# Performance work log

Hardware: AMD Instinct MI355X
Metric: run time of the kernel (lower is better)

## Reference

```python
import jax, jax.numpy as jnp
import numpy as np

B, C, H, W = 4, 64, 256, 256
HEADS, DHEAD = 4, 64
INNER = HEADS * DHEAD


def setup_inputs() -> dict:
    key = jax.random.key(0)
    ks = jax.random.split(key, 8)
    s = 1.0 / np.sqrt(C)
    return {
        "x_in": jax.random.normal(ks[0], (B, C, H, W), jnp.float32),
        "illu_fea_trans": jax.random.normal(ks[1], (B, C, H, W), jnp.float32),
        "Wq": jax.random.normal(ks[2], (C, INNER), jnp.float32) * s,
        "Wk": jax.random.normal(ks[3], (C, INNER), jnp.float32) * s,
        "Wv": jax.random.normal(ks[4], (C, INNER), jnp.float32) * s,
        "WL": jax.random.normal(ks[5], (C, INNER), jnp.float32) * s,
        "rescale": jnp.ones((HEADS, 1, 1), jnp.float32),
        "Wp": jax.random.normal(ks[6], (INNER, C), jnp.float32) / np.sqrt(INNER),
        "bp": jnp.zeros((C,), jnp.float32),
    }


def _l2norm(t, axis=-1, eps=1e-12):
    # matches torch F.normalize(p=2): x / max(||x||, eps)
    n = jnp.sqrt(jnp.sum(t * t, axis=axis, keepdims=True))
    return t / jnp.maximum(n, eps)


def reference(x_in, illu_fea_trans, Wq, Wk, Wv, WL, rescale, Wp, bp):
    b, c, h, w = x_in.shape
    n = h * w
    # NCHW -> [b, n, c]
    x = jnp.transpose(x_in, (0, 2, 3, 1)).reshape(b, n, c)
    illu = jnp.transpose(illu_fea_trans, (0, 2, 3, 1)).reshape(b, n, c)

    def split_heads(t):  # [b,n,inner] -> [b,heads,d,n] (transposed attention)
        return jnp.transpose(t.reshape(b, n, HEADS, DHEAD), (0, 2, 3, 1))

    q = split_heads(x @ Wq)           # [b,h,d,n]
    k = split_heads(x @ Wk)
    v = split_heads(x @ Wv) * split_heads(illu @ WL)  # illumination-gated v

    q = _l2norm(q, axis=-1)
    k = _l2norm(k, axis=-1)
    attn = jnp.einsum('bhdn,bhen->bhde', k, q)  # [b,h,d,d]
    attn = jax.nn.softmax(attn * rescale[None], axis=-1)
    out = jnp.einsum('bhde,bhen->bhdn', attn, v)  # [b,h,d,n]

    # [b,h,d,n] -> [b,n,inner]
    out = jnp.transpose(out, (0, 3, 1, 2)).reshape(b, n, INNER)
    out = out @ Wp + bp  # [b,n,c]
    return jnp.transpose(out.reshape(b, h, w, c), (0, 3, 1, 2))  # [b,c,h,w]
```

## Files before the change

### kernel.cpp

```cpp
#include <hip/hip_runtime.h>
#include <hip/hip_bf16.h>


#define NPOS 65536
#define CH 64
#define INNER 256

typedef __attribute__((ext_vector_type(8))) __bf16 bfrag;
typedef __attribute__((ext_vector_type(4))) float facc;
typedef __attribute__((ext_vector_type(4))) float fvec4;

__device__ __forceinline__ unsigned short f2bu(float f) {
  return __builtin_bit_cast(unsigned short, (__bf16)f);
}

#define SWA(row, colbyte) ((row) * 128 + ((colbyte) ^ (((row) & 7) << 4)))

__global__ __launch_bounds__(256) void k0_wt(const float* __restrict__ Wv,
                                             const float* __restrict__ WL,
                                             unsigned short* __restrict__ WvT,
                                             unsigned short* __restrict__ WLT) {
  int t = blockIdx.x * 256 + threadIdx.x;
  int c = t >> 8, i = t & 255;
  WvT[i * CH + c] = f2bu(Wv[c * INNER + i]);
  WLT[i * CH + c] = f2bu(WL[c * INNER + i]);
}

__global__ __launch_bounds__(256) void k1_xx(const float* __restrict__ x,
                                             float* __restrict__ xx) {
  const int b = blockIdx.y;
  const int wave = threadIdx.x >> 6, lane = threadIdx.x & 63;
  const int r = lane & 15, g = lane >> 4;
  const int gw = blockIdx.x * 4 + wave;
  const int per = NPOS / 128;
  const size_t n0 = (size_t)gw * per;
  const float* xb = x + (size_t)b * CH * NPOS;

  facc acc[4][4] = {};

  for (int n = 0; n < per; n += 32) {
    bfrag fr[4];
#pragma unroll
    for (int t = 0; t < 4; ++t) {
      const float* p = xb + (size_t)(16 * t + r) * NPOS + n0 + n + g * 8;
      fvec4 lo = *(const fvec4*)p;
      fvec4 hi = *(const fvec4*)(p + 4);
      bfrag f;
#pragma unroll
      for (int e = 0; e < 4; ++e) { f[e] = (__bf16)lo[e]; f[e + 4] = (__bf16)hi[e]; }
      fr[t] = f;
    }
#pragma unroll
    for (int ti = 0; ti < 4; ++ti)
#pragma unroll
      for (int tj = 0; tj < 4; ++tj)
        acc[ti][tj] = __builtin_amdgcn_mfma_f32_16x16x32_bf16(fr[ti], fr[tj],
                                                              acc[ti][tj], 0, 0, 0);
  }

  __shared__ float red[4][4096];
  float* my = red[wave];
#pragma unroll
  for (int ti = 0; ti < 4; ++ti)
#pragma unroll
    for (int tj = 0; tj < 4; ++tj)
#pragma unroll
      for (int q = 0; q < 4; ++q)
        my[(16 * ti + g * 4 + q) * 64 + 16 * tj + r] = acc[ti][tj][q];
  __syncthreads();
  float* xxb = xx + (size_t)b * 4096;
  for (int i = threadIdx.x; i < 4096; i += 256)
    atomicAdd(xxb + i, red[0][i] + red[1][i] + red[2][i] + red[3][i]);
}

__global__ __launch_bounds__(256) void k2_attn(
    const float* __restrict__ xx, const float* __restrict__ Wq,
    const float* __restrict__ Wk, const float* __restrict__ rescale,
    const float* __restrict__ Wp, unsigned short* __restrict__ Mt) {
  const int b = blockIdx.x >> 2, h = blockIdx.x & 3;
  const int t = threadIdx.x;
  const int wave = t >> 6, lane = t & 63;
  const int r = lane & 15, g = lane >> 4;

  __shared__ __align__(16) char tXX[8192];
  __shared__ __align__(16) char tWq[8192];
  __shared__ __align__(16) char tWk[8192];
  __shared__ __align__(16) char tWp[8192];
  __shared__ __align__(16) char tZq[8192];
  __shared__ __align__(16) char tZk[8192];
  __shared__ __align__(16) char tAt[8192];
  __shared__ float gG[64][68];
  __shared__ float sMx[64][4], sSm[64][4];
  __shared__ float sNq[64], sNk[64];

  const float* xxb = xx + (size_t)b * 4096;
#pragma unroll
  for (int rep = 0; rep < 16; ++rep) {
    int idx = rep * 256 + t;
    int row = idx >> 6, col = idx & 63;
    *(unsigned short*)(tXX + SWA(row, col * 2)) = f2bu(xxb[idx]);
    float vq = Wq[row * INNER + h * 64 + col];
    float vk = Wk[row * INNER + h * 64 + col];
    *(unsigned short*)(tWq + SWA(col, row * 2)) = f2bu(vq);
    *(unsigned short*)(tWk + SWA(col, row * 2)) = f2bu(vk);
    *(unsigned short*)(tWp + SWA(col, row * 2)) = f2bu(Wp[(h * 64 + row) * CH + col]);
  }
  __syncthreads();

  facc zq[4] = {}, zk[4] = {};
#pragma unroll
  for (int s = 0; s < 2; ++s) {
    bfrag aq = *(const bfrag*)(tWq + SWA(16 * wave + r, s * 64 + g * 16));
    bfrag ak = *(const bfrag*)(tWk + SWA(16 * wave + r, s * 64 + g * 16));
#pragma unroll
    for (int tj = 0; tj < 4; ++tj) {
      bfrag bx = *(const bfrag*)(tXX + SWA(16 * tj + r, s * 64 + g * 16));
      zq[tj] = __builtin_amdgcn_mfma_f32_16x16x32_bf16(aq, bx, zq[tj], 0, 0, 0);
      zk[tj] = __builtin_amdgcn_mfma_f32_16x16x32_bf16(ak, bx, zk[tj], 0, 0, 0);
    }
  }
#pragma unroll
  for (int tj = 0; tj < 4; ++tj)
#pragma unroll
    for (int q = 0; q < 4; ++q) {
      int row = 16 * wave + g * 4 + q, colb = (16 * tj + r) * 2;
      *(unsigned short*)(tZq + SWA(row, colb)) = f2bu(zq[tj][q]);
      *(unsigned short*)(tZk + SWA(row, colb)) = f2bu(zk[tj][q]);
    }
  __syncthreads();

  facc ga[4] = {}, q2[4] = {}, k2[4] = {};
#pragma unroll
  for (int s = 0; s < 2; ++s) {
    bfrag azk = *(const bfrag*)(tZk + SWA(16 * wave + r, s * 64 + g * 16));
    bfrag azq = *(const bfrag*)(tZq + SWA(16 * wave + r, s * 64 + g * 16));
#pragma unroll
    for (int tj = 0; tj < 4; ++tj) {
      bfrag bq = *(const bfrag*)(tWq + SWA(16 * tj + r, s * 64 + g * 16));
      bfrag bk = *(const bfrag*)(tWk + SWA(16 * tj + r, s * 64 + g * 16));
      ga[tj] = __builtin_amdgcn_mfma_f32_16x16x32_bf16(azk, bq, ga[tj], 0, 0, 0);
      q2[tj] = __builtin_amdgcn_mfma_f32_16x16x32_bf16(azq, bq, q2[tj], 0, 0, 0);
      k2[tj] = __builtin_amdgcn_mfma_f32_16x16x32_bf16(azk, bk, k2[tj], 0, 0, 0);
    }
  }
#pragma unroll
  for (int tj = 0; tj < 4; ++tj)
#pragma unroll
    for (int q = 0; q < 4; ++q) {
      int row = 16 * wave + g * 4 + q, col = 16 * tj + r;
      gG[row][col] = ga[tj][q];
      if (row == col) { sNq[row] = q2[tj][q]; sNk[row] = k2[tj][q]; }
    }
  __syncthreads();

  if (t < 64) {
    sNq[t] = 1.f / fmaxf(sqrtf(sNq[t]), 1e-12f);
    sNk[t] = rescale[h] / fmaxf(sqrtf(sNk[t]), 1e-12f);
  }
  __syncthreads();

  {
    const int d = t >> 2, p = t & 3;
    const float ik = sNk[d];
    float le[16];
    float mx = -1e30f;
#pragma unroll
    for (int j = 0; j < 16; ++j) {
      float v = gG[d][16 * p + j] * ik * sNq[16 * p + j];
      le[j] = v; mx = fmaxf(mx, v);
    }
    sMx[d][p] = mx;
    __syncthreads();
    mx = fmaxf(fmaxf(sMx[d][0], sMx[d][1]), fmaxf(sMx[d][2], sMx[d][3]));
    float sm = 0.f;
#pragma unroll
    for (int j = 0; j < 16; ++j) { le[j] = __expf(le[j] - mx); sm += le[j]; }
    sSm[d][p] = sm;
    __syncthreads();
    sm = sSm[d][0] + sSm[d][1] + sSm[d][2] + sSm[d][3];
    const float inv = 1.f / sm;
#pragma unroll
    for (int j = 0; j < 16; ++j) {
      int e = 16 * p + j;
      *(unsigned short*)(tAt + SWA(e, d * 2)) = f2bu(le[j] * inv);
    }
  }
  __syncthreads();

  facc m[4] = {};
#pragma unroll
  for (int s = 0; s < 2; ++s) {
    bfrag aa = *(const bfrag*)(tAt + SWA(16 * wave + r, s * 64 + g * 16));
#pragma unroll
    for (int tj = 0; tj < 4; ++tj) {
      bfrag bw = *(const bfrag*)(tWp + SWA(16 * tj + r, s * 64 + g * 16));
      m[tj] = __builtin_amdgcn_mfma_f32_16x16x32_bf16(aa, bw, m[tj], 0, 0, 0);
    }
  }
#pragma unroll
  for (int tj = 0; tj < 4; ++tj)
#pragma unroll
    for (int q = 0; q < 4; ++q) {
      int e = 16 * wave + g * 4 + q, c2 = 16 * tj + r;
      Mt[((size_t)(b * CH + c2)) * INNER + h * 64 + e] = f2bu(m[tj][q]);
    }
}

__global__ __launch_bounds__(256) void k3_out(
    const float* __restrict__ x, const float* __restrict__ illu,
    const unsigned short* __restrict__ WvT, const unsigned short* __restrict__ WLT,
    const unsigned short* __restrict__ Mt, const float* __restrict__ bp,
    float* __restrict__ out) {
  const int b = blockIdx.y;
  const int wave = threadIdx.x >> 6, lane = threadIdx.x & 63;
  const int r = lane & 15, g = lane >> 4;
  const int n0 = blockIdx.x * 256;

  __shared__ __align__(16) char lxs[8192];
  __shared__ __align__(16) char lis[8192];
  __shared__ __align__(16) char lvs[2][8192];

  bfrag wvA[4][2], wlA[4][2], mtA[8];
#pragma unroll
  for (int ti = 0; ti < 4; ++ti) {
    const int i = wave * 64 + ti * 16 + r;
#pragma unroll
    for (int s = 0; s < 2; ++s) {
      wvA[ti][s] = *(const bfrag*)(WvT + i * CH + s * 32 + g * 8);
      wlA[ti][s] = *(const bfrag*)(WLT + i * CH + s * 32 + g * 8);
    }
  }
#pragma unroll
  for (int s8 = 0; s8 < 8; ++s8)
    mtA[s8] = *(const bfrag*)(Mt + ((size_t)(b * CH + wave * 16 + r)) * INNER + s8 * 32 + g * 8);
  float bcol[4];
#pragma unroll
  for (int q = 0; q < 4; ++q) bcol[q] = bp[wave * 16 + g * 4 + q];

  const float* xb = x + (size_t)b * CH * NPOS;
  const float* ib = illu + (size_t)b * CH * NPOS;
  float* ob = out + (size_t)b * CH * NPOS;

  const int sc2 = threadIdx.x >> 3;
  const int sjo = (threadIdx.x & 7) * 8;

  for (int chunk = 0; chunk < 4; ++chunk) {
    const int nbase = n0 + chunk * 64;
    {
      const float* px0 = xb + (size_t)(2 * sc2) * NPOS + nbase + sjo;
      const float* pi0 = ib + (size_t)(2 * sc2) * NPOS + nbase + sjo;
      fvec4 xa0 = *(const fvec4*)px0,          xa1 = *(const fvec4*)(px0 + 4);
      fvec4 xb0 = *(const fvec4*)(px0 + NPOS), xb1 = *(const fvec4*)(px0 + NPOS + 4);
      fvec4 ia0 = *(const fvec4*)pi0,          ia1 = *(const fvec4*)(pi0 + 4);
      fvec4 ib0 = *(const fvec4*)(pi0 + NPOS), ib1 = *(const fvec4*)(pi0 + NPOS + 4);
#pragma unroll
      for (int jj = 0; jj < 8; ++jj) {
        const int j = sjo + jj;
        const int byte = (sc2 * 4) ^ (((j ^ (j >> 3)) & 7) << 4);
        float x0 = jj < 4 ? xa0[jj & 3] : xa1[jj & 3];
        float x1 = jj < 4 ? xb0[jj & 3] : xb1[jj & 3];
        float i0 = jj < 4 ? ia0[jj & 3] : ia1[jj & 3];
        float i1 = jj < 4 ? ib0[jj & 3] : ib1[jj & 3];
        *(unsigned int*)(lxs + j * 128 + byte) =
            (unsigned int)f2bu(x0) | ((unsigned int)f2bu(x1) << 16);
        *(unsigned int*)(lis + j * 128 + byte) =
            (unsigned int)f2bu(i0) | ((unsigned int)f2bu(i1) << 16);
      }
    }
    __syncthreads();

#pragma unroll
    for (int sub = 0; sub < 4; ++sub) {
      const int vb = sub & 1;
      const int j0 = sub * 16;
      const int j = j0 + r;
      const int swv = ((j ^ (j >> 3)) & 7) << 4;
      bfrag xB[2], iB[2];
#pragma unroll
      for (int s = 0; s < 2; ++s) {
        const int byte = (s * 64 + g * 16) ^ swv;
        xB[s] = *(const bfrag*)(lxs + j * 128 + byte);
        iB[s] = *(const bfrag*)(lis + j * 128 + byte);
      }
      facc av[4] = {}, gv[4] = {};
#pragma unroll
      for (int ti = 0; ti < 4; ++ti) {
#pragma unroll
        for (int s = 0; s < 2; ++s) {
          av[ti] = __builtin_amdgcn_mfma_f32_16x16x32_bf16(wvA[ti][s], xB[s], av[ti], 0, 0, 0);
          gv[ti] = __builtin_amdgcn_mfma_f32_16x16x32_bf16(wlA[ti][s], iB[s], gv[ti], 0, 0, 0);
        }
      }
#pragma unroll
      for (int ti = 0; ti < 4; ++ti) {
        const float v0 = av[ti][0] * gv[ti][0], v1 = av[ti][1] * gv[ti][1];
        const float v2 = av[ti][2] * gv[ti][2], v3 = av[ti][3] * gv[ti][3];
        const int i = wave * 64 + ti * 16 + g * 4;
        const int sw = (r & 7) << 4;
        *(unsigned int*)(lvs[vb] + r * 512 + ((i * 2) ^ sw)) =
            (unsigned int)f2bu(v0) | ((unsigned int)f2bu(v1) << 16);
        *(unsigned int*)(lvs[vb] + r * 512 + (((i + 2) * 2) ^ sw)) =
            (unsigned int)f2bu(v2) | ((unsigned int)f2bu(v3) << 16);
      }
      __syncthreads();
      facc ov = {0.f, 0.f, 0.f, 0.f};
#pragma unroll
      for (int s8 = 0; s8 < 8; ++s8) {
        const int byte = (s8 * 64 + g * 16) ^ ((r & 7) << 4);
        bfrag vB = *(const bfrag*)(lvs[vb] + r * 512 + byte);
        ov = __builtin_amdgcn_mfma_f32_16x16x32_bf16(mtA[s8], vB, ov, 0, 0, 0);
      }
#pragma unroll
      for (int q = 0; q < 4; ++q)
        ob[(size_t)(wave * 16 + g * 4 + q) * NPOS + nbase + j0 + r] = ov[q] + bcol[q];
    }
  }
}

extern "C" void kernel_launch(void* const* d_in, const int* in_sizes, int n_in,
                              void* d_out, int out_size, void* d_ws, size_t ws_size,
                              hipStream_t stream) {
  (void)in_sizes; (void)n_in; (void)out_size; (void)ws_size;
  const float* x    = (const float*)d_in[0];
  const float* illu = (const float*)d_in[1];
  const float* Wq   = (const float*)d_in[2];
  const float* Wk   = (const float*)d_in[3];
  const float* Wv   = (const float*)d_in[4];
  const float* WL   = (const float*)d_in[5];
  const float* rsc  = (const float*)d_in[6];
  const float* Wp   = (const float*)d_in[7];
  const float* bp   = (const float*)d_in[8];
  float* out = (float*)d_out;

  float* xxws = (float*)d_ws;
  unsigned short* Mt  = (unsigned short*)((char*)d_ws + 65536);
  unsigned short* WvT = (unsigned short*)((char*)d_ws + 65536 + 131072);
  unsigned short* WLT = WvT + INNER * CH;

  hipMemsetAsync(d_ws, 0, (size_t)4 * 4096 * sizeof(float), stream);
  hipLaunchKernelGGL(k0_wt, dim3(64), dim3(256), 0, stream, Wv, WL, WvT, WLT);
  hipLaunchKernelGGL(k1_xx, dim3(32, 4), dim3(256), 0, stream, x, xxws);
  hipLaunchKernelGGL(k2_attn, dim3(16), dim3(256), 0, stream, xxws, Wq, Wk, rsc, Wp, Mt);
  hipLaunchKernelGGL(k3_out, dim3(256, 4), dim3(256), 0, stream, x, illu, WvT, WLT, Mt, bp, out);
}
```

Measured before the change: 83.96 us.

## Double-buffer x/illu staging in k3_out with register prefetch and MFMA priority

```diff
diff --git a/kernel.cpp b/kernel.cpp
--- a/kernel.cpp
+++ b/kernel.cpp
@@ -206,7 +206,7 @@
     }
 }
 
-__global__ __launch_bounds__(256) void k3_out(
+__global__ __launch_bounds__(256, 3) void k3_out(
     const float* __restrict__ x, const float* __restrict__ illu,
     const unsigned short* __restrict__ WvT, const unsigned short* __restrict__ WLT,
     const unsigned short* __restrict__ Mt, const float* __restrict__ bp,
@@ -216,8 +216,8 @@
   const int r = lane & 15, g = lane >> 4;
   const int n0 = blockIdx.x * 256;
 
-  __shared__ __align__(16) char lxs[8192];
-  __shared__ __align__(16) char lis[8192];
+  __shared__ __align__(16) char lxs[2][8192];
+  __shared__ __align__(16) char lis[2][8192];
   __shared__ __align__(16) char lvs[2][8192];
 
   bfrag wvA[4][2], wlA[4][2], mtA[8];
@@ -244,30 +244,43 @@
   const int sc2 = threadIdx.x >> 3;
   const int sjo = (threadIdx.x & 7) * 8;
 
+  fvec4 xa0, xa1, xr0, xr1, ia0, ia1, ir0, ir1;
+
+#define LOADC(NB)                                                         \
+  {                                                                       \
+    const float* px0 = xb + (size_t)(2 * sc2) * NPOS + (NB) + sjo;        \
+    const float* pi0 = ib + (size_t)(2 * sc2) * NPOS + (NB) + sjo;        \
+    xa0 = *(const fvec4*)px0;          xa1 = *(const fvec4*)(px0 + 4);    \
+    xr0 = *(const fvec4*)(px0 + NPOS); xr1 = *(const fvec4*)(px0 + NPOS + 4); \
+    ia0 = *(const fvec4*)pi0;          ia1 = *(const fvec4*)(pi0 + 4);    \
+    ir0 = *(const fvec4*)(pi0 + NPOS); ir1 = *(const fvec4*)(pi0 + NPOS + 4); \
+  }
+
+#define WRITEC(BUF)                                                       \
+  {                                                                       \
+    _Pragma("unroll")                                                     \
+    for (int jj = 0; jj < 8; ++jj) {                                      \
+      const int j = sjo + jj;                                             \
+      const int byte = (sc2 * 4) ^ (((j ^ (j >> 3)) & 7) << 4);           \
+      float x0 = jj < 4 ? xa0[jj & 3] : xa1[jj & 3];                      \
+      float x1 = jj < 4 ? xr0[jj & 3] : xr1[jj & 3];                      \
+      float i0 = jj < 4 ? ia0[jj & 3] : ia1[jj & 3];                      \
+      float i1 = jj < 4 ? ir0[jj & 3] : ir1[jj & 3];                      \
+      *(unsigned int*)(lxs[BUF] + j * 128 + byte) =                       \
+          (unsigned int)f2bu(x0) | ((unsigned int)f2bu(x1) << 16);        \
+      *(unsigned int*)(lis[BUF] + j * 128 + byte) =                       \
+          (unsigned int)f2bu(i0) | ((unsigned int)f2bu(i1) << 16);        \
+    }                                                                     \
+  }
+
+  LOADC(n0);
+  WRITEC(0);
+  __syncthreads();
+
   for (int chunk = 0; chunk < 4; ++chunk) {
+    const int cb = chunk & 1;
     const int nbase = n0 + chunk * 64;
-    {
-      const float* px0 = xb + (size_t)(2 * sc2) * NPOS + nbase + sjo;
-      const float* pi0 = ib + (size_t)(2 * sc2) * NPOS + nbase + sjo;
-      fvec4 xa0 = *(const fvec4*)px0,          xa1 = *(const fvec4*)(px0 + 4);
-      fvec4 xb0 = *(const fvec4*)(px0 + NPOS), xb1 = *(const fvec4*)(px0 + NPOS + 4);
-      fvec4 ia0 = *(const fvec4*)pi0,          ia1 = *(const fvec4*)(pi0 + 4);
-      fvec4 ib0 = *(const fvec4*)(pi0 + NPOS), ib1 = *(const fvec4*)(pi0 + NPOS + 4);
-#pragma unroll
-      for (int jj = 0; jj < 8; ++jj) {
-        const int j = sjo + jj;
-        const int byte = (sc2 * 4) ^ (((j ^ (j >> 3)) & 7) << 4);
-        float x0 = jj < 4 ? xa0[jj & 3] : xa1[jj & 3];
-        float x1 = jj < 4 ? xb0[jj & 3] : xb1[jj & 3];
-        float i0 = jj < 4 ? ia0[jj & 3] : ia1[jj & 3];
-        float i1 = jj < 4 ? ib0[jj & 3] : ib1[jj & 3];
-        *(unsigned int*)(lxs + j * 128 + byte) =
-            (unsigned int)f2bu(x0) | ((unsigned int)f2bu(x1) << 16);
-        *(unsigned int*)(lis + j * 128 + byte) =
-            (unsigned int)f2bu(i0) | ((unsigned int)f2bu(i1) << 16);
-      }
-    }
-    __syncthreads();
+    if (chunk < 3) LOADC(nbase + 64);
 
 #pragma unroll
     for (int sub = 0; sub < 4; ++sub) {
@@ -279,10 +292,11 @@
 #pragma unroll
       for (int s = 0; s < 2; ++s) {
         const int byte = (s * 64 + g * 16) ^ swv;
-        xB[s] = *(const bfrag*)(lxs + j * 128 + byte);
-        iB[s] = *(const bfrag*)(lis + j * 128 + byte);
+        xB[s] = *(const bfrag*)(lxs[cb] + j * 128 + byte);
+        iB[s] = *(const bfrag*)(lis[cb] + j * 128 + byte);
       }
       facc av[4] = {}, gv[4] = {};
+      __builtin_amdgcn_s_setprio(1);
 #pragma unroll
       for (int ti = 0; ti < 4; ++ti) {
 #pragma unroll
@@ -291,6 +305,7 @@
           gv[ti] = __builtin_amdgcn_mfma_f32_16x16x32_bf16(wlA[ti][s], iB[s], gv[ti], 0, 0, 0);
         }
       }
+      __builtin_amdgcn_s_setprio(0);
 #pragma unroll
       for (int ti = 0; ti < 4; ++ti) {
         const float v0 = av[ti][0] * gv[ti][0], v1 = av[ti][1] * gv[ti][1];
@@ -304,17 +319,24 @@
       }
       __syncthreads();
       facc ov = {0.f, 0.f, 0.f, 0.f};
+      __builtin_amdgcn_s_setprio(1);
 #pragma unroll
       for (int s8 = 0; s8 < 8; ++s8) {
         const int byte = (s8 * 64 + g * 16) ^ ((r & 7) << 4);
         bfrag vB = *(const bfrag*)(lvs[vb] + r * 512 + byte);
         ov = __builtin_amdgcn_mfma_f32_16x16x32_bf16(mtA[s8], vB, ov, 0, 0, 0);
       }
+      __builtin_amdgcn_s_setprio(0);
 #pragma unroll
       for (int q = 0; q < 4; ++q)
         ob[(size_t)(wave * 16 + g * 4 + q) * NPOS + nbase + j0 + r] = ov[q] + bcol[q];
     }
-  }
+
+    if (chunk < 3) WRITEC(cb ^ 1);
+    __syncthreads();
+  }
+#undef LOADC
+#undef WRITEC
 }
 
 extern "C" void kernel_launch(void* const* d_in, const int* in_sizes, int n_in,
```

Result: slower. 208.6 us (+148.5%).

## Restructure output kernel so each wave owns positions and chains MFMA without LDS round-trip

Applied to the files above, without the earlier changes.

```diff
diff --git a/kernel.cpp b/kernel.cpp
--- a/kernel.cpp
+++ b/kernel.cpp
@@ -9,10 +9,22 @@
 typedef __attribute__((ext_vector_type(8))) __bf16 bfrag;
 typedef __attribute__((ext_vector_type(4))) float facc;
 typedef __attribute__((ext_vector_type(4))) float fvec4;
+typedef __attribute__((ext_vector_type(4))) short sh4;
 
 __device__ __forceinline__ unsigned short f2bu(float f) {
   return __builtin_bit_cast(unsigned short, (__bf16)f);
 }
+
+#if __has_builtin(__builtin_amdgcn_mfma_f32_16x16x16bf16_1k)
+__device__ __forceinline__ facc mfma16(sh4 a, sh4 b, facc c) {
+  return __builtin_amdgcn_mfma_f32_16x16x16bf16_1k(a, b, c, 0, 0, 0);
+}
+#else
+__device__ __forceinline__ facc mfma16(sh4 a, sh4 b, facc c) {
+  asm("v_mfma_f32_16x16x16_bf16 %0, %1, %2, %0" : "+v"(c) : "v"(a), "v"(b));
+  return c;
+}
+#endif
 
 #define SWA(row, colbyte) ((row) * 128 + ((colbyte) ^ (((row) & 7) << 4)))
 
@@ -76,7 +88,7 @@
 __global__ __launch_bounds__(256) void k2_attn(
     const float* __restrict__ xx, const float* __restrict__ Wq,
     const float* __restrict__ Wk, const float* __restrict__ rescale,
-    const float* __restrict__ Wp, unsigned short* __restrict__ Mt) {
+    const float* __restrict__ Wp, unsigned short* __restrict__ Mt3) {
   const int b = blockIdx.x >> 2, h = blockIdx.x & 3;
   const int t = threadIdx.x;
   const int wave = t >> 6, lane = t & 63;
@@ -201,118 +213,90 @@
   for (int tj = 0; tj < 4; ++tj)
 #pragma unroll
     for (int q = 0; q < 4; ++q) {
-      int e = 16 * wave + g * 4 + q, c2 = 16 * tj + r;
-      Mt[((size_t)(b * CH + c2)) * INNER + h * 64 + e] = f2bu(m[tj][q]);
+      int i_glob = h * 64 + 16 * wave + g * 4 + q;
+      int c2 = 16 * tj + r;
+      Mt3[((size_t)b * 16 + (i_glob >> 4)) * 1024 + c2 * 16 + (i_glob & 15)] =
+          f2bu(m[tj][q]);
     }
 }
 
 __global__ __launch_bounds__(256) void k3_out(
     const float* __restrict__ x, const float* __restrict__ illu,
     const unsigned short* __restrict__ WvT, const unsigned short* __restrict__ WLT,
-    const unsigned short* __restrict__ Mt, const float* __restrict__ bp,
+    const unsigned short* __restrict__ Mt3, const float* __restrict__ bp,
     float* __restrict__ out) {
   const int b = blockIdx.y;
   const int wave = threadIdx.x >> 6, lane = threadIdx.x & 63;
   const int r = lane & 15, g = lane >> 4;
-  const int n0 = blockIdx.x * 256;
-
-  __shared__ __align__(16) char lxs[8192];
-  __shared__ __align__(16) char lis[8192];
-  __shared__ __align__(16) char lvs[2][8192];
-
-  bfrag wvA[4][2], wlA[4][2], mtA[8];
-#pragma unroll
-  for (int ti = 0; ti < 4; ++ti) {
-    const int i = wave * 64 + ti * 16 + r;
+  const int n0 = blockIdx.x * 256 + wave * 64;
+
+  __shared__ __align__(16) char sst[4][2][2048];
+  char* myx = sst[wave][0];
+  char* myi = sst[wave][1];
+
+  const float* xb = x + (size_t)b * CH * NPOS + (size_t)lane * NPOS;
+  const float* ib = illu + (size_t)b * CH * NPOS + (size_t)lane * NPOS;
+  float* ob = out + (size_t)b * CH * NPOS;
+  const unsigned short* mt = Mt3 + (size_t)b * 16384;
+
+  float bias[4];
+#pragma unroll
+  for (int ct = 0; ct < 4; ++ct) bias[ct] = bp[ct * 16 + r];
+
+  for (int t = 0; t < 4; ++t) {
+    const int nb = n0 + t * 16;
+    {
+      fvec4 xv[4], iv[4];
+#pragma unroll
+      for (int p = 0; p < 4; ++p) {
+        xv[p] = *(const fvec4*)(xb + nb + p * 4);
+        iv[p] = *(const fvec4*)(ib + nb + p * 4);
+      }
+#pragma unroll
+      for (int j = 0; j < 16; ++j) {
+        const int byte = (lane * 2) ^ ((j & 7) << 4);
+        *(unsigned short*)(myx + j * 128 + byte) = f2bu(xv[j >> 2][j & 3]);
+        *(unsigned short*)(myi + j * 128 + byte) = f2bu(iv[j >> 2][j & 3]);
+      }
+    }
+    bfrag xB[2], iB[2];
 #pragma unroll
     for (int s = 0; s < 2; ++s) {
-      wvA[ti][s] = *(const bfrag*)(WvT + i * CH + s * 32 + g * 8);
-      wlA[ti][s] = *(const bfrag*)(WLT + i * CH + s * 32 + g * 8);
-    }
-  }
-#pragma unroll
-  for (int s8 = 0; s8 < 8; ++s8)
-    mtA[s8] = *(const bfrag*)(Mt + ((size_t)(b * CH + wave * 16 + r)) * INNER + s8 * 32 + g * 8);
-  float bcol[4];
-#pragma unroll
-  for (int q = 0; q < 4; ++q) bcol[q] = bp[wave * 16 + g * 4 + q];
-
-  const float* xb = x + (size_t)b * CH * NPOS;
-  const float* ib = illu + (size_t)b * CH * NPOS;
-  float* ob = out + (size_t)b * CH * NPOS;
-
-  const int sc2 = threadIdx.x >> 3;
-  const int sjo = (threadIdx.x & 7) * 8;
-
-  for (int chunk = 0; chunk < 4; ++chunk) {
-    const int nbase = n0 + chunk * 64;
-    {
-      const float* px0 = xb + (size_t)(2 * sc2) * NPOS + nbase + sjo;
-      const float* pi0 = ib + (size_t)(2 * sc2) * NPOS + nbase + sjo;
-      fvec4 xa0 = *(const fvec4*)px0,          xa1 = *(const fvec4*)(px0 + 4);
-      fvec4 xb0 = *(const fvec4*)(px0 + NPOS), xb1 = *(const fvec4*)(px0 + NPOS + 4);
-      fvec4 ia0 = *(const fvec4*)pi0,          ia1 = *(const fvec4*)(pi0 + 4);
-      fvec4 ib0 = *(const fvec4*)(pi0 + NPOS), ib1 = *(const fvec4*)(pi0 + NPOS + 4);
-#pragma unroll
-      for (int jj = 0; jj < 8; ++jj) {
-        const int j = sjo + jj;
-        const int byte = (sc2 * 4) ^ (((j ^ (j >> 3)) & 7) << 4);
-        float x0 = jj < 4 ? xa0[jj & 3] : xa1[jj & 3];
-        float x1 = jj < 4 ? xb0[jj & 3] : xb1[jj & 3];
-        float i0 = jj < 4 ? ia0[jj & 3] : ia1[jj & 3];
-        float i1 = jj < 4 ? ib0[jj & 3] : ib1[jj & 3];
-        *(unsigned int*)(lxs + j * 128 + byte) =
-            (unsigned int)f2bu(x0) | ((unsigned int)f2bu(x1) << 16);
-        *(unsigned int*)(lis + j * 128 + byte) =
-            (unsigned int)f2bu(i0) | ((unsigned int)f2bu(i1) << 16);
+      const int byte = (s * 64 + g * 16) ^ ((r & 7) << 4);
+      xB[s] = *(const bfrag*)(myx + r * 128 + byte);
+      iB[s] = *(const bfrag*)(myi + r * 128 + byte);
+    }
+
+    facc acc[4] = {};
+#pragma unroll 4
+    for (int ti = 0; ti < 16; ++ti) {
+      const int irow = ti * 16 + r;
+      bfrag wv0 = *(const bfrag*)(WvT + irow * CH + g * 8);
+      bfrag wv1 = *(const bfrag*)(WvT + irow * CH + 32 + g * 8);
+      bfrag wl0 = *(const bfrag*)(WLT + irow * CH + g * 8);
+      bfrag wl1 = *(const bfrag*)(WLT + irow * CH + 32 + g * 8);
+      facc av = {}, gv = {};
+      av = __builtin_amdgcn_mfma_f32_16x16x32_bf16(wv0, xB[0], av, 0, 0, 0);
+      av = __builtin_amdgcn_mfma_f32_16x16x32_bf16(wv1, xB[1], av, 0, 0, 0);
+      gv = __builtin_amdgcn_mfma_f32_16x16x32_bf16(wl0, iB[0], gv, 0, 0, 0);
+      gv = __builtin_amdgcn_mfma_f32_16x16x32_bf16(wl1, iB[1], gv, 0, 0, 0);
+      sh4 a2;
+#pragma unroll
+      for (int e = 0; e < 4; ++e)
+        a2[e] = (short)f2bu(av[e] * gv[e]);
+      const unsigned short* mrow = mt + ti * 1024 + g * 4;
+#pragma unroll
+      for (int ct = 0; ct < 4; ++ct) {
+        sh4 mb = *(const sh4*)(mrow + (ct * 16 + r) * 16);
+        acc[ct] = mfma16(a2, mb, acc[ct]);
       }
     }
-    __syncthreads();
-
-#pragma unroll
-    for (int sub = 0; sub < 4; ++sub) {
-      const int vb = sub & 1;
-      const int j0 = sub * 16;
-      const int j = j0 + r;
-      const int swv = ((j ^ (j >> 3)) & 7) << 4;
-      bfrag xB[2], iB[2];
-#pragma unroll
-      for (int s = 0; s < 2; ++s) {
-        const int byte = (s * 64 + g * 16) ^ swv;
-        xB[s] = *(const bfrag*)(lxs + j * 128 + byte);
-        iB[s] = *(const bfrag*)(lis + j * 128 + byte);
-      }
-      facc av[4] = {}, gv[4] = {};
-#pragma unroll
-      for (int ti = 0; ti < 4; ++ti) {
-#pragma unroll
-        for (int s = 0; s < 2; ++s) {
-          av[ti] = __builtin_amdgcn_mfma_f32_16x16x32_bf16(wvA[ti][s], xB[s], av[ti], 0, 0, 0);
-          gv[ti] = __builtin_amdgcn_mfma_f32_16x16x32_bf16(wlA[ti][s], iB[s], gv[ti], 0, 0, 0);
-        }
-      }
-#pragma unroll
-      for (int ti = 0; ti < 4; ++ti) {
-        const float v0 = av[ti][0] * gv[ti][0], v1 = av[ti][1] * gv[ti][1];
-        const float v2 = av[ti][2] * gv[ti][2], v3 = av[ti][3] * gv[ti][3];
-        const int i = wave * 64 + ti * 16 + g * 4;
-        const int sw = (r & 7) << 4;
-        *(unsigned int*)(lvs[vb] + r * 512 + ((i * 2) ^ sw)) =
-            (unsigned int)f2bu(v0) | ((unsigned int)f2bu(v1) << 16);
-        *(unsigned int*)(lvs[vb] + r * 512 + (((i + 2) * 2) ^ sw)) =
-            (unsigned int)f2bu(v2) | ((unsigned int)f2bu(v3) << 16);
-      }
-      __syncthreads();
-      facc ov = {0.f, 0.f, 0.f, 0.f};
-#pragma unroll
-      for (int s8 = 0; s8 < 8; ++s8) {
-        const int byte = (s8 * 64 + g * 16) ^ ((r & 7) << 4);
-        bfrag vB = *(const bfrag*)(lvs[vb] + r * 512 + byte);
-        ov = __builtin_amdgcn_mfma_f32_16x16x32_bf16(mtA[s8], vB, ov, 0, 0, 0);
-      }
-#pragma unroll
-      for (int q = 0; q < 4; ++q)
-        ob[(size_t)(wave * 16 + g * 4 + q) * NPOS + nbase + j0 + r] = ov[q] + bcol[q];
+#pragma unroll
+    for (int ct = 0; ct < 4; ++ct) {
+      fvec4 o;
+#pragma unroll
+      for (int q = 0; q < 4; ++q) o[q] = acc[ct][q] + bias[ct];
+      *(fvec4*)(ob + (size_t)(ct * 16 + r) * NPOS + nb + g * 4) = o;
     }
   }
 }
@@ -333,13 +317,13 @@
   float* out = (float*)d_out;
 
   float* xxws = (float*)d_ws;
-  unsigned short* Mt  = (unsigned short*)((char*)d_ws + 65536);
+  unsigned short* Mt3 = (unsigned short*)((char*)d_ws + 65536);
   unsigned short* WvT = (unsigned short*)((char*)d_ws + 65536 + 131072);
   unsigned short* WLT = WvT + INNER * CH;
 
   hipMemsetAsync(d_ws, 0, (size_t)4 * 4096 * sizeof(float), stream);
   hipLaunchKernelGGL(k0_wt, dim3(64), dim3(256), 0, stream, Wv, WL, WvT, WLT);
   hipLaunchKernelGGL(k1_xx, dim3(32, 4), dim3(256), 0, stream, x, xxws);
-  hipLaunchKernelGGL(k2_attn, dim3(16), dim3(256), 0, stream, xxws, Wq, Wk, rsc, Wp, Mt);
-  hipLaunchKernelGGL(k3_out, dim3(256, 4), dim3(256), 0, stream, x, illu, WvT, WLT, Mt, bp, out);
-}
+  hipLaunchKernelGGL(k2_attn, dim3(16), dim3(256), 0, stream, xxws, Wq, Wk, rsc, Wp, Mt3);
+  hipLaunchKernelGGL(k3_out, dim3(256, 4), dim3(256), 0, stream, x, illu, WvT, WLT, Mt3, bp, out);
+}
```

Measured after the change: 209.2 us. 149% more time.

## Double-buffer k3 input tiles via async global-to-LDS loads

Applied to the files above, without the earlier changes.

```diff
diff --git a/kernel.cpp b/kernel.cpp
--- a/kernel.cpp
+++ b/kernel.cpp
@@ -10,11 +10,18 @@
 typedef __attribute__((ext_vector_type(4))) float facc;
 typedef __attribute__((ext_vector_type(4))) float fvec4;
 
+typedef const __attribute__((address_space(1))) unsigned int guint;
+typedef __attribute__((address_space(3))) unsigned int luint;
+
 __device__ __forceinline__ unsigned short f2bu(float f) {
   return __builtin_bit_cast(unsigned short, (__bf16)f);
 }
 
 #define SWA(row, colbyte) ((row) * 128 + ((colbyte) ^ (((row) & 7) << 4)))
+
+#define BAR_VM4()  asm volatile("s_waitcnt vmcnt(4)\n\ts_barrier" ::: "memory")
+#define BAR_VM0()  asm volatile("s_waitcnt vmcnt(0)\n\ts_barrier" ::: "memory")
+#define BAR_LGKM() asm volatile("s_waitcnt lgkmcnt(0)\n\ts_barrier" ::: "memory")
 
 __global__ __launch_bounds__(256) void k0_wt(const float* __restrict__ Wv,
                                              const float* __restrict__ WL,
@@ -216,8 +223,8 @@
   const int r = lane & 15, g = lane >> 4;
   const int n0 = blockIdx.x * 256;
 
-  __shared__ __align__(16) char lxs[8192];
-  __shared__ __align__(16) char lis[8192];
+  __shared__ __align__(16) float xf[2][64][32];
+  __shared__ __align__(16) float ifl[2][64][32];
   __shared__ __align__(16) char lvs[2][8192];
 
   bfrag wvA[4][2], wlA[4][2], mtA[8];
@@ -241,48 +248,58 @@
   const float* ib = illu + (size_t)b * CH * NPOS;
   float* ob = out + (size_t)b * CH * NPOS;
 
-  const int sc2 = threadIdx.x >> 3;
-  const int sjo = (threadIdx.x & 7) * 8;
-
-  for (int chunk = 0; chunk < 4; ++chunk) {
-    const int nbase = n0 + chunk * 64;
-    {
-      const float* px0 = xb + (size_t)(2 * sc2) * NPOS + nbase + sjo;
-      const float* pi0 = ib + (size_t)(2 * sc2) * NPOS + nbase + sjo;
-      fvec4 xa0 = *(const fvec4*)px0,          xa1 = *(const fvec4*)(px0 + 4);
-      fvec4 xb0 = *(const fvec4*)(px0 + NPOS), xb1 = *(const fvec4*)(px0 + NPOS + 4);
-      fvec4 ia0 = *(const fvec4*)pi0,          ia1 = *(const fvec4*)(pi0 + 4);
-      fvec4 ib0 = *(const fvec4*)(pi0 + NPOS), ib1 = *(const fvec4*)(pi0 + NPOS + 4);
-#pragma unroll
-      for (int jj = 0; jj < 8; ++jj) {
-        const int j = sjo + jj;
-        const int byte = (sc2 * 4) ^ (((j ^ (j >> 3)) & 7) << 4);
-        float x0 = jj < 4 ? xa0[jj & 3] : xa1[jj & 3];
-        float x1 = jj < 4 ? xb0[jj & 3] : xb1[jj & 3];
-        float i0 = jj < 4 ? ia0[jj & 3] : ia1[jj & 3];
-        float i1 = jj < 4 ? ib0[jj & 3] : ib1[jj & 3];
-        *(unsigned int*)(lxs + j * 128 + byte) =
-            (unsigned int)f2bu(x0) | ((unsigned int)f2bu(x1) << 16);
-        *(unsigned int*)(lis + j * 128 + byte) =
-            (unsigned int)f2bu(i0) | ((unsigned int)f2bu(i1) << 16);
-      }
-    }
-    __syncthreads();
-
-#pragma unroll
-    for (int sub = 0; sub < 4; ++sub) {
-      const int vb = sub & 1;
+  const int c0 = wave * 16 + (lane >> 3);
+  const int c1 = c0 + 8;
+  const int k0_ = (c0 >> 3) & 3, k1_ = (c1 >> 3) & 3;
+  const int fk0 = k0_ ^ ((k0_ & 1) << 2), fk1 = k1_ ^ ((k1_ & 1) << 2);
+  const size_t off0 = (size_t)c0 * NPOS + (((lane & 7) ^ fk0) << 2);
+  const size_t off1 = (size_t)c1 * NPOS + (((lane & 7) ^ fk1) << 2);
+
+#define ISSUE(BUF, NC)                                                        \
+  {                                                                           \
+    __builtin_amdgcn_global_load_lds((guint*)(xb + off0 + (NC)),              \
+        (luint*)&xf[BUF][wave * 16][0], 16, 0, 0);                            \
+    __builtin_amdgcn_global_load_lds((guint*)(xb + off1 + (NC)),              \
+        (luint*)&xf[BUF][wave * 16 + 8][0], 16, 0, 0);                        \
+    __builtin_amdgcn_global_load_lds((guint*)(ib + off0 + (NC)),              \
+        (luint*)&ifl[BUF][wave * 16][0], 16, 0, 0);                           \
+    __builtin_amdgcn_global_load_lds((guint*)(ib + off1 + (NC)),              \
+        (luint*)&ifl[BUF][wave * 16 + 8][0], 16, 0, 0);                       \
+  }
+
+  ISSUE(0, n0);
+  BAR_VM0();
+
+  const int fkr = g ^ ((g & 1) << 2);
+
+  for (int cc = 0; cc < 8; ++cc) {
+    const int cb = cc & 1;
+    const int nbase = n0 + cc * 32;
+    if (cc < 7) ISSUE(cb ^ 1, nbase + 32);
+    BAR_VM4();
+
+#pragma unroll 2
+    for (int sub = 0; sub < 2; ++sub) {
       const int j0 = sub * 16;
       const int j = j0 + r;
-      const int swv = ((j ^ (j >> 3)) & 7) << 4;
+      const int qw = ((((j >> 2) ^ fkr) << 2) | (j & 3));
       bfrag xB[2], iB[2];
 #pragma unroll
       for (int s = 0; s < 2; ++s) {
-        const int byte = (s * 64 + g * 16) ^ swv;
-        xB[s] = *(const bfrag*)(lxs + j * 128 + byte);
-        iB[s] = *(const bfrag*)(lis + j * 128 + byte);
+        float xw[8], iw[8];
+#pragma unroll
+        for (int e = 0; e < 8; ++e) {
+          const int c = s * 32 + g * 8 + e;
+          xw[e] = xf[cb][c][qw];
+          iw[e] = ifl[cb][c][qw];
+        }
+        bfrag fx, fi;
+#pragma unroll
+        for (int e = 0; e < 8; ++e) { fx[e] = (__bf16)xw[e]; fi[e] = (__bf16)iw[e]; }
+        xB[s] = fx; iB[s] = fi;
       }
       facc av[4] = {}, gv[4] = {};
+      __builtin_amdgcn_s_setprio(1);
 #pragma unroll
       for (int ti = 0; ti < 4; ++ti) {
 #pragma unroll
@@ -291,30 +308,34 @@
           gv[ti] = __builtin_amdgcn_mfma_f32_16x16x32_bf16(wlA[ti][s], iB[s], gv[ti], 0, 0, 0);
         }
       }
+      __builtin_amdgcn_s_setprio(0);
 #pragma unroll
       for (int ti = 0; ti < 4; ++ti) {
         const float v0 = av[ti][0] * gv[ti][0], v1 = av[ti][1] * gv[ti][1];
         const float v2 = av[ti][2] * gv[ti][2], v3 = av[ti][3] * gv[ti][3];
         const int i = wave * 64 + ti * 16 + g * 4;
         const int sw = (r & 7) << 4;
-        *(unsigned int*)(lvs[vb] + r * 512 + ((i * 2) ^ sw)) =
-            (unsigned int)f2bu(v0) | ((unsigned int)f2bu(v1) << 16);
-        *(unsigned int*)(lvs[vb] + r * 512 + (((i + 2) * 2) ^ sw)) =
-            (unsigned int)f2bu(v2) | ((unsigned int)f2bu(v3) << 16);
+        unsigned long long pk =
+            (unsigned long long)((unsigned int)f2bu(v0) | ((unsigned int)f2bu(v1) << 16)) |
+            ((unsigned long long)((unsigned int)f2bu(v2) | ((unsigned int)f2bu(v3) << 16)) << 32);
+        *(unsigned long long*)(lvs[sub] + r * 512 + ((i * 2) ^ sw)) = pk;
       }
-      __syncthreads();
+      BAR_LGKM();
       facc ov = {0.f, 0.f, 0.f, 0.f};
+      __builtin_amdgcn_s_setprio(1);
 #pragma unroll
       for (int s8 = 0; s8 < 8; ++s8) {
         const int byte = (s8 * 64 + g * 16) ^ ((r & 7) << 4);
-        bfrag vB = *(const bfrag*)(lvs[vb] + r * 512 + byte);
+        bfrag vB = *(const bfrag*)(lvs[sub] + r * 512 + byte);
         ov = __builtin_amdgcn_mfma_f32_16x16x32_bf16(mtA[s8], vB, ov, 0, 0, 0);
       }
+      __builtin_amdgcn_s_setprio(0);
 #pragma unroll
       for (int q = 0; q < 4; ++q)
         ob[(size_t)(wave * 16 + g * 4 + q) * NPOS + nbase + j0 + r] = ov[q] + bcol[q];
     }
   }
+#undef ISSUE
 }
 
 extern "C" void kernel_launch(void* const* d_in, const int* in_sizes, int n_in,
```

Result: no change. 85.48 us (+1.8%).
